# Performance work log

Hardware: AMD Instinct MI355X
Metric: run time of the kernel (lower is better)

## Reference

```python
import jax, jax.numpy as jnp
import numpy as np
import math

NWIN = (16, 16)   # windows per side
P = 8             # win_patch
STRIDE = 4        # shift
H = 8             # num_head
HID = 128         # hidden_dim (per-head dim)
C = 128           # input_dim (== hidden_dim)
N = P * P         # tokens per window = 64
SDK = math.sqrt(HID)


def setup_inputs() -> dict:
    key = jax.random.key(0)
    ks = jax.random.split(key, 11)
    s = 0.02
    return {
        "x": jax.random.normal(ks[0], (NWIN[0] * NWIN[1] * 4, N, C), jnp.float32),
        "mask": jax.random.uniform(ks[1], (3, N, N), jnp.float32),
        "Bp": jax.random.normal(ks[2], (N, N), jnp.float32),
        "wq_w": jax.random.normal(ks[3], (H * HID, C), jnp.float32) * s,
        "wq_b": jax.random.normal(ks[4], (H * HID,), jnp.float32) * s,
        "wk_w": jax.random.normal(ks[5], (H * HID, C), jnp.float32) * s,
        "wk_b": jax.random.normal(ks[6], (H * HID,), jnp.float32) * s,
        "wv_w": jax.random.normal(ks[7], (H * HID, C), jnp.float32) * s,
        "wv_b": jax.random.normal(ks[8], (H * HID,), jnp.float32) * s,
        "proj_w": jax.random.normal(ks[9], (C, H * HID), jnp.float32) * s,
        "proj_b": jax.random.normal(ks[10], (C,), jnp.float32) * s,
    }


def reference(x, mask, Bp, wq_w, wq_b, wk_w, wk_b, wv_w, wv_b, proj_w, proj_b):
    nh, nw = NWIN
    b = x.shape[0] // (nh * nw)

    # windows -> full image, shift by (-stride, -stride), re-partition
    img = x.reshape(b, nh, nw, P, P, C).transpose(0, 1, 3, 2, 4, 5)
    img = img.reshape(b, nh * P, nw * P, C)
    img = jnp.roll(img, (-STRIDE, -STRIDE), axis=(1, 2))
    xw = img.reshape(b, nh, P, nw, P, C).transpose(0, 1, 3, 2, 4, 5).reshape(-1, N, C)

    q = xw @ wq_w.T + wq_b
    k = xw @ wk_w.T + wk_b
    v = xw @ wv_w.T + wv_b
    Bw = q.shape[0]  # total windows
    q = q.reshape(Bw, N, H, HID).transpose(0, 2, 1, 3)
    k = k.reshape(Bw, N, H, HID).transpose(0, 2, 1, 3)
    v = v.reshape(Bw, N, H, HID).transpose(0, 2, 1, 3)

    att = jnp.einsum("bhnd,bhmd->bhnm", q, k) / jnp.asarray(SDK, q.dtype) + Bp
    att = jax.nn.softmax(att, axis=-1)

    # border-window multiplicative mask (interior windows pass through)
    att = att.reshape(b, nh, nw, H, N, N)
    wmask = jnp.ones((nh, nw, 1, N, N), dtype=att.dtype)
    wmask = wmask.at[-1, :-1].set(mask[0])   # bottom row (except corner)
    wmask = wmask.at[:-1, -1].set(mask[1])   # right column (except corner)
    wmask = wmask.at[-1, -1].set(mask[2])    # bottom-right corner
    att = (att * wmask[None]).reshape(Bw, H, N, N)

    out = jnp.einsum("bhnm,bhmd->bhnd", att, v)
    out = out.transpose(0, 2, 1, 3).reshape(Bw, N, H * HID)
    out = out @ proj_w.T + proj_b

    # reverse shift and re-partition into windows
    img = out.reshape(b, nh, nw, P, P, C).transpose(0, 1, 3, 2, 4, 5)
    img = img.reshape(b, nh * P, nw * P, C)
    img = jnp.roll(img, (STRIDE, STRIDE), axis=(1, 2))
    return img.reshape(b, nh, P, nw, P, C).transpose(0, 1, 3, 2, 4, 5).reshape(-1, N, C)
```

## Files before the change

### kernel.cpp

```cpp
#include <hip/hip_runtime.h>
#include <hip/hip_bf16.h>

typedef __attribute__((ext_vector_type(8))) short bf16x8;
typedef __attribute__((ext_vector_type(4))) float f32x4;

#define LXW  0
#define LT   16384
#define LV   32768
#define LATT 49152
#define LRW  57344

__device__ __forceinline__ int sw256(int o){ return o ^ (((o >> 8) & 7) << 4); }
__device__ __forceinline__ int sw128(int o){ return o ^ (((o >> 7) & 7) << 4); }

__device__ __forceinline__ short f2bf(float f){
  union { float f; unsigned u; } v; v.f = f;
  unsigned r = v.u + 0x7FFFu + ((v.u >> 16) & 1u);
  return (short)(r >> 16);
}
__device__ __forceinline__ float bf2f(short s){
  union { unsigned u; float f; } v; v.u = ((unsigned)(unsigned short)s) << 16;
  return v.f;
}
__device__ __forceinline__ bf16x8 lds8(const char* smem, int off){
  return *(const bf16x8*)(smem + off);
}

__global__ void wfused_k(const float* __restrict__ pw, const float* __restrict__ wv,
                         const float* __restrict__ wv_b,
                         short* __restrict__ wf, float* __restrict__ bf) {
  int blk = blockIdx.x;
  int h = blk >> 7, co = blk & 127;
  int ci = threadIdx.x;
  const float* pr = pw + (size_t)co * 1024 + h * 128;
  const float* wr = wv + (size_t)h * 128 * 128 + ci;
  float acc = 0.f;
#pragma unroll 4
  for (int d = 0; d < 128; ++d)
    acc += pr[d] * wr[(size_t)d * 128];
  wf[(size_t)h * 16384 + co * 128 + ci] = f2bf(acc);
  if (ci < 64) {
    float b = wv_b[h*128 + ci] * pr[ci] + wv_b[h*128 + 64 + ci] * pr[64 + ci];
    b += __shfl_xor(b, 1);  b += __shfl_xor(b, 2);  b += __shfl_xor(b, 4);
    b += __shfl_xor(b, 8);  b += __shfl_xor(b, 16); b += __shfl_xor(b, 32);
    if (ci == 0) bf[h*128 + co] = b;
  }
}

__global__ void mt_k(const float* __restrict__ wq, const float* __restrict__ wk,
                     const float* __restrict__ bq, const float* __restrict__ bk,
                     short* __restrict__ mt, float* __restrict__ uarr,
                     float* __restrict__ varr, float* __restrict__ carr) {
  int blk = blockIdx.x;
  int h = blk >> 7, kp = blk & 127;
  int ci = threadIdx.x;
  const float* wkc = wk + (size_t)h * 16384 + kp;
  const float* wqc = wq + (size_t)h * 16384 + ci;
  float macc = 0.f, vacc = 0.f;
#pragma unroll 4
  for (int d = 0; d < 128; ++d) {
    float wqv = wqc[(size_t)d * 128];
    macc += wkc[(size_t)d * 128] * wqv;
    vacc += bk[h*128 + d] * wqv;
  }
  mt[(size_t)h * 16384 + kp * 128 + ci] = f2bf(macc);
  if (ci == 0) {
    float u = 0.f;
#pragma unroll 4
    for (int d = 0; d < 128; ++d) u += bq[h*128 + d] * wkc[(size_t)d * 128];
    uarr[h*128 + kp] = u;
  }
  if (kp == 0) {
    varr[h*128 + ci] = vacc;
    if (ci == 0) {
      float c = 0.f;
#pragma unroll 4
      for (int d = 0; d < 128; ++d) c += bq[h*128 + d] * bk[h*128 + d];
      carr[h] = c;
    }
  }
}

__global__ __launch_bounds__(256, 2) void swattn_main(
    const float* __restrict__ x, const float* __restrict__ mask,
    const float* __restrict__ Bp, const float* __restrict__ proj_b,
    const short* __restrict__ mt, const short* __restrict__ wfz,
    const float* __restrict__ uarr, const float* __restrict__ bfu,
    const float* __restrict__ varr, const float* __restrict__ carr,
    float* __restrict__ out)
{
  __shared__ alignas(16) char smem[59392];
  const int tid  = threadIdx.x;
  const int wvid = tid >> 6, lane = tid & 63, lr = lane & 15, lg = lane >> 4;
  const int rbp  = (wvid >> 1) * 2;
  const int jh   = wvid & 1;
  const int wid = blockIdx.x;
  const int bb = wid >> 8, wy = (wid >> 4) & 15, wx = wid & 15;

  {
    int token = tid >> 2, q = tid & 3;
    int py = token >> 3, px = token & 7;
    int Y = (wy*8 + py + 4) & 127;
    int X = (wx*8 + px + 4) & 127;
    int swin = bb*256 + ((Y>>3)<<4) + (X>>3);
    int stok = ((Y&7)<<3) + (X&7);
    const float* src = x + ((size_t)(swin*64 + stok))*128 + q*32;
    int base = LXW + token*256 + q*64;
#pragma unroll
    for (int j = 0; j < 32; j += 8) {
      float4 f0 = *(const float4*)(src + j);
      float4 f1 = *(const float4*)(src + j + 4);
      bf16x8 bv;
      bv[0]=f2bf(f0.x); bv[1]=f2bf(f0.y); bv[2]=f2bf(f0.z); bv[3]=f2bf(f0.w);
      bv[4]=f2bf(f1.x); bv[5]=f2bf(f1.y); bv[6]=f2bf(f1.z); bv[7]=f2bf(f1.w);
      *(bf16x8*)(smem + sw256(base + j*2)) = bv;
    }
  }
  __syncthreads();

  bf16x8 af[2][4];
#pragma unroll
  for (int r2 = 0; r2 < 2; ++r2) {
    int arow = (rbp + r2)*16 + lr;
#pragma unroll
    for (int kk = 0; kk < 4; ++kk)
      af[r2][kk] = *(const bf16x8*)(smem + sw256(LXW + arow*256 + kk*64 + lg*16));
  }

#pragma unroll
  for (int e2 = 0; e2 < 2; ++e2) {
    int e = tid*2 + e2;
    int h = e >> 6, i = e & 63;
    float acc = carr[h];
#pragma unroll
    for (int k8 = 0; k8 < 16; ++k8) {
      bf16x8 xv = lds8(smem, sw256(LXW + i*256 + k8*16));
      float4 va = *(const float4*)(varr + h*128 + k8*8);
      float4 vb = *(const float4*)(varr + h*128 + k8*8 + 4);
      acc += bf2f(xv[0])*va.x + bf2f(xv[1])*va.y + bf2f(xv[2])*va.z + bf2f(xv[3])*va.w;
      acc += bf2f(xv[4])*vb.x + bf2f(xv[5])*vb.y + bf2f(xv[6])*vb.z + bf2f(xv[7])*vb.w;
    }
    *(float*)(smem + LRW + e*4) = acc;
  }
  __syncthreads();

  const float* mrow = nullptr;
  if (wy == 15 && wx != 15)      mrow = mask;
  else if (wx == 15 && wy != 15) mrow = mask + 4096;
  else if (wy == 15 && wx == 15) mrow = mask + 8192;
  float bpv[4][4], mv[4][4];
  {
    int i0 = 16*wvid + lg*4;
#pragma unroll
    for (int cb = 0; cb < 4; ++cb)
#pragma unroll
      for (int rr = 0; rr < 4; ++rr) {
        bpv[cb][rr] = Bp[(i0+rr)*64 + cb*16 + lr];
        mv[cb][rr]  = mrow ? mrow[(i0+rr)*64 + cb*16 + lr] : 1.0f;
      }
  }

  f32x4 accO[8];
#pragma unroll
  for (int ct = 0; ct < 8; ++ct) accO[ct] = f32x4{0.f, 0.f, 0.f, 0.f};

  const float isdk = 0.088388347648318447f;

  for (int h = 0; h < 8; ++h) {
    {
      const short* wmat[2] = { mt, wfz };
      const float* bvec[2] = { uarr, bfu };
#pragma unroll
      for (int s = 0; s < 2; ++s) {
#pragma unroll
        for (int t = 0; t < 4; ++t) {
          int j = (jh*4 + t)*16 + lr;
          const short* wr = wmat[s] + (size_t)(h*128 + j)*128;
          bf16x8 bfv[4];
#pragma unroll
          for (int kk = 0; kk < 4; ++kk)
            bfv[kk] = *(const bf16x8*)(wr + kk*32 + lg*8);
          float bias = bvec[s][h*128 + j];
#pragma unroll
          for (int r2 = 0; r2 < 2; ++r2) {
            int rb = rbp + r2;
            f32x4 acc = f32x4{0.f,0.f,0.f,0.f};
#pragma unroll
            for (int kk = 0; kk < 4; ++kk)
              acc = __builtin_amdgcn_mfma_f32_16x16x32_bf16(af[r2][kk], bfv[kk], acc, 0,0,0);
            if (s == 0) {
#pragma unroll
              for (int rr = 0; rr < 4; ++rr) {
                int row = rb*16 + lg*4 + rr;
                *(short*)(smem + sw256(LT + row*256 + j*2)) = f2bf(acc[rr] + bias);
              }
            } else {
              short4 p;
              p.x = f2bf(acc[0] + bias); p.y = f2bf(acc[1] + bias);
              p.z = f2bf(acc[2] + bias); p.w = f2bf(acc[3] + bias);
              int m0 = rb*16 + lg*4;
              *(short4*)(smem + sw128(LV + j*128 + m0*2)) = p;
            }
          }
        }
      }
    }
    __syncthreads();

    {
      float pv[4][4];
      bf16x8 qf[4];
      int qrow = 16*wvid + lr;
#pragma unroll
      for (int kk = 0; kk < 4; ++kk)
        qf[kk] = *(const bf16x8*)(smem + sw256(LT + qrow*256 + kk*64 + lg*16));
      int i0 = 16*wvid + lg*4;
      float rwb[4];
#pragma unroll
      for (int rr = 0; rr < 4; ++rr)
        rwb[rr] = *(const float*)(smem + LRW + (h*64 + i0 + rr)*4) * isdk;
      __builtin_amdgcn_s_setprio(1);
#pragma unroll
      for (int cb = 0; cb < 4; ++cb) {
        f32x4 at = f32x4{0.f,0.f,0.f,0.f};
        int krow = cb*16 + lr;
#pragma unroll
        for (int kk = 0; kk < 4; ++kk) {
          bf16x8 kf = *(const bf16x8*)(smem + sw256(LXW + krow*256 + kk*64 + lg*16));
          at = __builtin_amdgcn_mfma_f32_16x16x32_bf16(qf[kk], kf, at, 0,0,0);
        }
#pragma unroll
        for (int rr = 0; rr < 4; ++rr)
          pv[cb][rr] = at[rr]*isdk + rwb[rr] + bpv[cb][rr];
      }
      __builtin_amdgcn_s_setprio(0);
#pragma unroll
      for (int rr = 0; rr < 4; ++rr) {
        float m = fmaxf(fmaxf(pv[0][rr], pv[1][rr]), fmaxf(pv[2][rr], pv[3][rr]));
        m = fmaxf(m, __shfl_xor(m, 1));
        m = fmaxf(m, __shfl_xor(m, 2));
        m = fmaxf(m, __shfl_xor(m, 4));
        m = fmaxf(m, __shfl_xor(m, 8));
        float s = 0.f;
#pragma unroll
        for (int cb = 0; cb < 4; ++cb) { pv[cb][rr] = __expf(pv[cb][rr] - m); s += pv[cb][rr]; }
        s += __shfl_xor(s, 1); s += __shfl_xor(s, 2);
        s += __shfl_xor(s, 4); s += __shfl_xor(s, 8);
        float inv = 1.0f / s;
#pragma unroll
        for (int cb = 0; cb < 4; ++cb) pv[cb][rr] = pv[cb][rr]*inv*mv[cb][rr];
      }
#pragma unroll
      for (int cb = 0; cb < 4; ++cb) {
        int mcol = cb*16 + lr;
#pragma unroll
        for (int rr = 0; rr < 4; ++rr)
          *(short*)(smem + sw128(LATT + (i0+rr)*128 + mcol*2)) = f2bf(pv[cb][rr]);
      }
    }

    {
      bf16x8 paf[2];
#pragma unroll
      for (int kk = 0; kk < 2; ++kk)
        paf[kk] = lds8(smem, sw128(LATT + (16*wvid + lr)*128 + kk*64 + lg*16));
      __builtin_amdgcn_s_setprio(1);
#pragma unroll
      for (int ct = 0; ct < 8; ++ct) {
        int d = ct*16 + lr;
#pragma unroll
        for (int kk = 0; kk < 2; ++kk) {
          bf16x8 vf = lds8(smem, sw128(LV + d*128 + kk*64 + lg*16));
          accO[ct] = __builtin_amdgcn_mfma_f32_16x16x32_bf16(paf[kk], vf, accO[ct], 0,0,0);
        }
      }
      __builtin_amdgcn_s_setprio(0);
    }
    __syncthreads();
  }

#pragma unroll
  for (int rr = 0; rr < 4; ++rr) {
    int i = 16*wvid + lg*4 + rr;
    int py = i >> 3, px = i & 7;
    int Y = (wy*8 + py + 4) & 127;
    int X = (wx*8 + px + 4) & 127;
    int dwin = bb*256 + ((Y>>3)<<4) + (X>>3);
    int dtok = ((Y&7)<<3) + (X&7);
    float* dst = out + ((size_t)(dwin*64 + dtok))*128;
#pragma unroll
    for (int ct = 0; ct < 8; ++ct)
      dst[ct*16 + lr] = accO[ct][rr] + proj_b[ct*16 + lr];
  }
}

extern "C" void kernel_launch(void* const* d_in, const int* in_sizes, int n_in,
                              void* d_out, int out_size, void* d_ws, size_t ws_size,
                              hipStream_t stream) {
  (void)in_sizes; (void)n_in; (void)out_size; (void)ws_size;
  const float* x      = (const float*)d_in[0];
  const float* mask   = (const float*)d_in[1];
  const float* Bp     = (const float*)d_in[2];
  const float* wq_w   = (const float*)d_in[3];
  const float* wq_b   = (const float*)d_in[4];
  const float* wk_w   = (const float*)d_in[5];
  const float* wk_b   = (const float*)d_in[6];
  const float* wv_w   = (const float*)d_in[7];
  const float* wv_b   = (const float*)d_in[8];
  const float* proj_w = (const float*)d_in[9];
  const float* proj_b = (const float*)d_in[10];
  float* out = (float*)d_out;
  short* wsb  = (short*)d_ws;
  short* wfz  = wsb;
  short* mt   = wsb + 131072;
  float* bfu  = (float*)(wsb + 262144);
  float* uarr = bfu + 1024;
  float* varr = bfu + 2048;
  float* carr = bfu + 3072;

  wfused_k<<<1024, 128, 0, stream>>>(proj_w, wv_w, wv_b, wfz, bfu);
  mt_k<<<1024, 128, 0, stream>>>(wq_w, wk_w, wq_b, wk_b, mt, uarr, varr, carr);
  swattn_main<<<1024, 256, 0, stream>>>(x, mask, Bp, proj_b,
      mt, wfz, uarr, bfu, varr, carr, out);
}
```

Baseline: 199.8 us.

## Fold softmax scale into precomputed weights and batch weight loads per head

Moves the 1/sqrt(d) scaling into the weight-preprocessing kernel, so the fused QK matrix and its bias vectors arrive pre-scaled and the main kernel skips a multiply per score. Also restructures the per-head projection loop to issue all 16 global weight-fragment loads and biases for a stage before any MFMA, so memory latency overlaps with compute. Batching the loads raises register pressure and may threaten the two-blocks-per-CU occupancy target.

Result: slower. 234.6 us (+17.4%).

```diff
diff --git a/kernel.cpp b/kernel.cpp
--- a/kernel.cpp
+++ b/kernel.cpp
@@ -51,6 +51,7 @@
                      const float* __restrict__ bq, const float* __restrict__ bk,
                      short* __restrict__ mt, float* __restrict__ uarr,
                      float* __restrict__ varr, float* __restrict__ carr) {
+  const float isdk = 0.088388347648318447f;
   int blk = blockIdx.x;
   int h = blk >> 7, kp = blk & 127;
   int ci = threadIdx.x;
@@ -63,20 +64,20 @@
     macc += wkc[(size_t)d * 128] * wqv;
     vacc += bk[h*128 + d] * wqv;
   }
-  mt[(size_t)h * 16384 + kp * 128 + ci] = f2bf(macc);
+  mt[(size_t)h * 16384 + kp * 128 + ci] = f2bf(macc * isdk);
   if (ci == 0) {
     float u = 0.f;
 #pragma unroll 4
     for (int d = 0; d < 128; ++d) u += bq[h*128 + d] * wkc[(size_t)d * 128];
-    uarr[h*128 + kp] = u;
+    uarr[h*128 + kp] = u * isdk;
   }
   if (kp == 0) {
-    varr[h*128 + ci] = vacc;
+    varr[h*128 + ci] = vacc * isdk;
     if (ci == 0) {
       float c = 0.f;
 #pragma unroll 4
       for (int d = 0; d < 128; ++d) c += bq[h*128 + d] * bk[h*128 + d];
-      carr[h] = c;
+      carr[h] = c * isdk;
     }
   }
 }
@@ -164,43 +165,45 @@
 #pragma unroll
   for (int ct = 0; ct < 8; ++ct) accO[ct] = f32x4{0.f, 0.f, 0.f, 0.f};
 
-  const float isdk = 0.088388347648318447f;
-
   for (int h = 0; h < 8; ++h) {
-    {
-      const short* wmat[2] = { mt, wfz };
-      const float* bvec[2] = { uarr, bfu };
-#pragma unroll
-      for (int s = 0; s < 2; ++s) {
-#pragma unroll
-        for (int t = 0; t < 4; ++t) {
-          int j = (jh*4 + t)*16 + lr;
-          const short* wr = wmat[s] + (size_t)(h*128 + j)*128;
-          bf16x8 bfv[4];
+#pragma unroll
+    for (int s = 0; s < 2; ++s) {
+      const short* wbase = s ? wfz : mt;
+      const float* bbase = s ? bfu : uarr;
+      bf16x8 bfvA[4][4];
+      float biasA[4];
+#pragma unroll
+      for (int t = 0; t < 4; ++t) {
+        int j = (jh*4 + t)*16 + lr;
+        const short* wr = wbase + (size_t)(h*128 + j)*128;
+#pragma unroll
+        for (int kk = 0; kk < 4; ++kk)
+          bfvA[t][kk] = *(const bf16x8*)(wr + kk*32 + lg*8);
+        biasA[t] = bbase[h*128 + j];
+      }
+#pragma unroll
+      for (int t = 0; t < 4; ++t) {
+        int j = (jh*4 + t)*16 + lr;
+        float bias = biasA[t];
+#pragma unroll
+        for (int r2 = 0; r2 < 2; ++r2) {
+          int rb = rbp + r2;
+          f32x4 acc = f32x4{0.f,0.f,0.f,0.f};
 #pragma unroll
           for (int kk = 0; kk < 4; ++kk)
-            bfv[kk] = *(const bf16x8*)(wr + kk*32 + lg*8);
-          float bias = bvec[s][h*128 + j];
-#pragma unroll
-          for (int r2 = 0; r2 < 2; ++r2) {
-            int rb = rbp + r2;
-            f32x4 acc = f32x4{0.f,0.f,0.f,0.f};
-#pragma unroll
-            for (int kk = 0; kk < 4; ++kk)
-              acc = __builtin_amdgcn_mfma_f32_16x16x32_bf16(af[r2][kk], bfv[kk], acc, 0,0,0);
-            if (s == 0) {
-#pragma unroll
-              for (int rr = 0; rr < 4; ++rr) {
-                int row = rb*16 + lg*4 + rr;
-                *(short*)(smem + sw256(LT + row*256 + j*2)) = f2bf(acc[rr] + bias);
-              }
-            } else {
-              short4 p;
-              p.x = f2bf(acc[0] + bias); p.y = f2bf(acc[1] + bias);
-              p.z = f2bf(acc[2] + bias); p.w = f2bf(acc[3] + bias);
-              int m0 = rb*16 + lg*4;
-              *(short4*)(smem + sw128(LV + j*128 + m0*2)) = p;
+            acc = __builtin_amdgcn_mfma_f32_16x16x32_bf16(af[r2][kk], bfvA[t][kk], acc, 0,0,0);
+          if (s == 0) {
+#pragma unroll
+            for (int rr = 0; rr < 4; ++rr) {
+              int row = rb*16 + lg*4 + rr;
+              *(short*)(smem + sw256(LT + row*256 + j*2)) = f2bf(acc[rr] + bias);
             }
+          } else {
+            short4 p;
+            p.x = f2bf(acc[0] + bias); p.y = f2bf(acc[1] + bias);
+            p.z = f2bf(acc[2] + bias); p.w = f2bf(acc[3] + bias);
+            int m0 = rb*16 + lg*4;
+            *(short4*)(smem + sw128(LV + j*128 + m0*2)) = p;
           }
         }
       }
@@ -218,7 +221,7 @@
       float rwb[4];
 #pragma unroll
       for (int rr = 0; rr < 4; ++rr)
-        rwb[rr] = *(const float*)(smem + LRW + (h*64 + i0 + rr)*4) * isdk;
+        rwb[rr] = *(const float*)(smem + LRW + (h*64 + i0 + rr)*4);
       __builtin_amdgcn_s_setprio(1);
 #pragma unroll
       for (int cb = 0; cb < 4; ++cb) {
@@ -231,7 +234,7 @@
         }
 #pragma unroll
         for (int rr = 0; rr < 4; ++rr)
-          pv[cb][rr] = at[rr]*isdk + rwb[rr] + bpv[cb][rr];
+          pv[cb][rr] = at[rr] + rwb[rr] + bpv[cb][rr];
       }
       __builtin_amdgcn_s_setprio(0);
 #pragma unroll
```
